# Performance work log

Measured on AMD Instinct MI355X. Metric: run time of the kernel, lower is better.

The kernel has to match this reference:

```python
import jax, jax.numpy as jnp
import numpy as np

N_NODES = 100000
N_EDGES = 1600000
N_GRAPHS = 1000
NODES_PER_GRAPH = 100
D_IN = 128
D_HID = 128
N_TASKS = 12


def setup_inputs() -> dict:
    key = jax.random.key(0)
    ks = jax.random.split(key, 6)
    X = jax.random.normal(ks[0], (N_NODES, D_IN), dtype=jnp.float32)
    edge_index = jax.random.randint(ks[1], (2, N_EDGES), 0, N_NODES, dtype=jnp.int64)
    graph_sizes = jnp.full((N_GRAPHS,), NODES_PER_GRAPH, dtype=jnp.int64)  # sums to N_NODES
    s0 = (2.0 / D_IN) ** 0.5
    W0 = jax.random.normal(ks[2], (D_IN, D_HID), dtype=jnp.float32) * s0
    b0 = jnp.zeros((D_HID,), dtype=jnp.float32)
    W1 = jax.random.normal(ks[3], (D_HID, D_HID), dtype=jnp.float32) * s0
    b1 = jnp.zeros((D_HID,), dtype=jnp.float32)
    Wf = jax.random.normal(ks[4], (D_HID, N_TASKS), dtype=jnp.float32) * s0
    bf = jnp.zeros((N_TASKS,), dtype=jnp.float32)
    return {"X": X, "edge_index": edge_index, "graph_sizes": graph_sizes,
            "W0": W0, "b0": b0, "W1": W1, "b1": b1, "Wf": Wf, "bf": bf}


def reference(X, edge_index, graph_sizes, W0, b0, W1, b1, Wf, bf):
    src, dst = edge_index[0], edge_index[1]
    n = X.shape[0]

    def gconv(x, W, b):
        # GCN-style message passing with self term: sum_{j->i} (x_j W) + x_i W + b
        xw = x @ W                                                    # [N, d]
        agg = jax.ops.segment_sum(xw[src], dst, num_segments=n)       # [N, d]
        return agg + xw + b

    # stacked conv -> relu -> dropout(eval=identity)
    h = jax.nn.relu(gconv(X, W0, b0))
    h = jax.nn.relu(gconv(h, W1, b1))
    out = jax.nn.sigmoid(h @ Wf + bf)                                  # [N, T]

    # ragged per-graph mean readout as a single segment-mean
    g = graph_sizes.shape[0]
    seg_ids = jnp.repeat(jnp.arange(g), graph_sizes, total_repeat_length=n)
    sums = jax.ops.segment_sum(out, seg_ids, num_segments=g)           # [G, T]
    return sums / graph_sizes[:, None].astype(out.dtype)
```

## Files before the change

### kernel.cpp

```cpp
#include <hip/hip_runtime.h>
#include <math.h>

#define D 128
#define NBUCK_MAX 1024
#define NB_EDGE   256
#define CAPSEG    40
#define CAPB      4096
#define CAPE      2600

typedef unsigned short u16;
typedef unsigned int   u32;
typedef __attribute__((ext_vector_type(8))) short short8;
typedef __attribute__((ext_vector_type(4))) float f32x4;
typedef __attribute__((ext_vector_type(2))) float f32x2;

static __device__ __forceinline__ u16 f32_to_bf16(float f) {
    u32 u = __builtin_bit_cast(u32, f);
    u32 r = (u + 0x7FFFu + ((u >> 16) & 1u)) >> 16;
    return (u16)r;
}
static __device__ __forceinline__ u32 pack_bf16x2(float lo, float hi) {
    return (u32)f32_to_bf16(lo) | ((u32)f32_to_bf16(hi) << 16);
}
static __device__ __forceinline__ float bf16lo_to_f32(u32 v) {
    return __builtin_bit_cast(float, v << 16);
}
static __device__ __forceinline__ float bf16hi_to_f32(u32 v) {
    return __builtin_bit_cast(float, v & 0xFFFF0000u);
}

__global__ __launch_bounds__(512) void prep_place(const int* __restrict__ src, const int* __restrict__ dst,
                                                  int E, int nbuck,
                                                  u32* __restrict__ edgeBuf, int* __restrict__ segCount,
                                                  const float* __restrict__ W0, const float* __restrict__ W1,
                                                  u16* __restrict__ Wp0, u16* __restrict__ Wp1,
                                                  const float* __restrict__ Wf, float* __restrict__ Wfp,
                                                  const int* __restrict__ gsz, int G, int* __restrict__ goff) {
    const int b = blockIdx.x;
    const int tid = threadIdx.x;
    if (b < NB_EDGE) {
        __shared__ int cur[NBUCK_MAX];
        for (int i = tid; i < nbuck; i += 512) cur[i] = 0;
        __syncthreads();
        int per = (E + NB_EDGE - 1) / NB_EDGE;
        int s = b * per, e = min(E, s + per);
        for (int i = s + tid; i < e; i += 512) {
            int d = dst[i];
            int bk = d >> 7;
            int pos = atomicAdd(&cur[bk], 1);
            if (pos < CAPSEG)
                edgeBuf[((size_t)bk * NB_EDGE + b) * CAPSEG + pos] = (u32)src[i] | ((u32)(d & 127) << 20);
        }
        __syncthreads();
        for (int i = tid; i < nbuck; i += 512) segCount[b * nbuck + i] = min(cur[i], CAPSEG);
    } else if (b == NB_EDGE) {
        __shared__ int wsum[8];
        int base = tid * 4;
        int v[4];
        #pragma unroll
        for (int k = 0; k < 4; k++) v[k] = (base + k < G) ? gsz[base + k] : 0;
        int s = v[0] + v[1] + v[2] + v[3];
        int lane = tid & 63;
        int incl = s;
        #pragma unroll
        for (int off = 1; off < 64; off <<= 1) { int t = __shfl_up(incl, off); if (lane >= off) incl += t; }
        int wv = tid >> 6;
        if (lane == 63) wsum[wv] = incl;
        __syncthreads();
        int woff = 0;
        for (int w = 0; w < wv; w++) woff += wsum[w];
        int run = woff + incl - s;
        #pragma unroll
        for (int k = 0; k < 4; k++) {
            if (base + k <= G) goff[base + k] = run;
            run += v[k];
        }
    } else if (b == NB_EDGE + 1) {
        for (int i = tid; i < 64 * 24; i += 512) {
            int lane = i / 24, r = i % 24, k = r / 3, j = r % 3;
            Wfp[i] = Wf[(((lane & 15) * 8) + k) * 12 + 3 * (lane >> 4) + j];
        }
    } else {
        int gidx = (b - (NB_EDGE + 2)) * 512 + tid;
        const float* W = (gidx < 128 * 128) ? W0 : W1;
        u16* Wp = (gidx < 128 * 128) ? Wp0 : Wp1;
        int idx = gidx & (128 * 128 - 1);
        int j = idx & 7, lane = (idx >> 3) & 63, kt = (idx >> 9) & 3, nt = idx >> 11;
        int k = kt * 32 + ((lane >> 4) << 3) + j;
        int n = nt * 16 + (lane & 15);
        Wp[idx] = f32_to_bf16(W[k * 128 + n]);
    }
}

static __device__ __forceinline__ void gemm_body(const short8 af[4], const u16* __restrict__ Wp,
                                                 u16* __restrict__ outb, int N, int row0,
                                                 int tid, int wave, int lane, int quad, int l16,
                                                 u16* Cs) {
    f32x4 acc[8];
    #pragma unroll
    for (int nt = 0; nt < 8; nt++) acc[nt] = (f32x4){0.f, 0.f, 0.f, 0.f};
    #pragma unroll
    for (int kt = 0; kt < 4; kt++) {
        #pragma unroll
        for (int nt = 0; nt < 8; nt++) {
            short8 bf = *(const short8*)(Wp + ((size_t)(nt * 4 + kt) * 64 + lane) * 8);
            acc[nt] = __builtin_amdgcn_mfma_f32_16x16x32_bf16(af[kt], bf, acc[nt], 0, 0, 0);
        }
    }
    #pragma unroll
    for (int nt = 0; nt < 8; nt++) {
        #pragma unroll
        for (int r = 0; r < 4; r++) {
            int rl = wave * 16 + quad * 4 + r;
            Cs[rl * 136 + nt * 16 + l16] = f32_to_bf16(acc[nt][r]);
        }
    }
    __syncthreads();
    for (int i = tid; i < 64 * 16; i += 256) {
        int row = i >> 4, chunk = i & 15;
        int grow = row0 + row;
        if (grow <= N)
            *(uint4*)(outb + (size_t)grow * 128 + chunk * 8) =
                *(const uint4*)(Cs + row * 136 + chunk * 8);
    }
}

__global__ __launch_bounds__(256) void finalize_gemm0(const u32* __restrict__ edgeBuf,
                                                      const int* __restrict__ segCount,
                                                      int2* __restrict__ rowse, int* __restrict__ col_idx,
                                                      int nbuck,
                                                      const float* __restrict__ A, const u16* __restrict__ Wp,
                                                      u16* __restrict__ outb, int N) {
    __shared__ u16 Cs[64 * 136];
    const int tid = threadIdx.x;
    if ((int)blockIdx.x < nbuck) {
        int* iCs   = (int*)Cs;
        u32* eL    = (u32*)iCs;
        int* hist  = iCs + CAPE;
        int* lcur  = iCs + CAPE + 128;
        int* scnt  = iCs + CAPE + 256;
        int* sbase = iCs + CAPE + 512;
        const int b = blockIdx.x;
        const size_t ebase = (size_t)b * NB_EDGE * CAPSEG;
        for (int i = tid; i < NB_EDGE; i += 256) scnt[i] = segCount[i * nbuck + b];
        if (tid < 128) hist[tid] = 0;
        __syncthreads();
        if (tid < 64) {
            int carry = 0;
            #pragma unroll
            for (int c4 = 0; c4 < NB_EDGE / 64; c4++) {
                int v = scnt[c4 * 64 + tid];
                int incl = v;
                #pragma unroll
                for (int off = 1; off < 64; off <<= 1) { int t = __shfl_up(incl, off); if (tid >= off) incl += t; }
                sbase[c4 * 64 + tid] = carry + incl - v;
                carry += __shfl(incl, 63);
            }
            if (tid == 0) sbase[NB_EDGE] = carry;
        }
        __syncthreads();
        const int nE = min(sbase[NB_EDGE], CAPE);
        for (int p = tid; p < nE; p += 256) {
            int lo = 0, hi = NB_EDGE;
            #pragma unroll
            for (int s = 0; s < 8; s++) {
                int mid = (lo + hi) >> 1;
                if (sbase[mid] <= p) lo = mid; else hi = mid;
            }
            eL[p] = edgeBuf[ebase + (size_t)lo * CAPSEG + (p - sbase[lo])];
        }
        __syncthreads();
        for (int i = tid; i < nE; i += 256)
            atomicAdd(&hist[(int)(eL[i] >> 20)], 1);
        __syncthreads();
        if (tid < 64) {
            int v0 = hist[tid * 2], v1 = hist[tid * 2 + 1];
            int s = v0 + v1;
            int incl = s;
            #pragma unroll
            for (int off = 1; off < 64; off <<= 1) { int t = __shfl_up(incl, off); if (tid >= off) incl += t; }
            int excl = incl - s;
            int le0 = excl + tid * 2;
            int le1 = le0 + v0 + 1;
            lcur[tid * 2]     = le0 + 1;
            lcur[tid * 2 + 1] = le1 + 1;
            int node = b * 128 + tid * 2;
            int st0 = b * CAPB + le0, st1 = b * CAPB + le1;
            if (node < N)     { rowse[node]     = make_int2(st0, st1);          col_idx[st0] = node; }
            if (node + 1 < N) { rowse[node + 1] = make_int2(st1, st1 + v1 + 1); col_idx[st1] = node + 1; }
        }
        __syncthreads();
        for (int i = tid; i < nE; i += 256) {
            u32 p = eL[i];
            int pos = atomicAdd(&lcur[p >> 20], 1);
            col_idx[b * CAPB + pos] = (int)(p & 0xFFFFFu);
        }
    } else {
        const int bid = blockIdx.x - nbuck;
        const int wave = tid >> 6, lane = tid & 63, quad = lane >> 4, l16 = lane & 15;
        const int row0 = bid * 64;
        const int arow = row0 + wave * 16 + l16;
        union { u32 u[4]; short8 s; } cv;
        short8 af[4];
        if (arow < N) {
            const float* ab = A + (size_t)arow * 128 + quad * 8;
            #pragma unroll
            for (int kt = 0; kt < 4; kt++) {
                float4 x0 = *(const float4*)(ab + kt * 32);
                float4 x1 = *(const float4*)(ab + kt * 32 + 4);
                cv.u[0] = pack_bf16x2(x0.x, x0.y);
                cv.u[1] = pack_bf16x2(x0.z, x0.w);
                cv.u[2] = pack_bf16x2(x1.x, x1.y);
                cv.u[3] = pack_bf16x2(x1.z, x1.w);
                af[kt] = cv.s;
            }
        } else {
            short8 z = {0, 0, 0, 0, 0, 0, 0, 0};
            #pragma unroll
            for (int kt = 0; kt < 4; kt++) af[kt] = z;
        }
        gemm_body(af, Wp, outb, N, row0, tid, wave, lane, quad, l16, Cs);
    }
}

static __device__ __forceinline__ void add_row(f32x2* acc, uint4 u) {
    acc[0] += (f32x2){bf16lo_to_f32(u.x), bf16hi_to_f32(u.x)};
    acc[1] += (f32x2){bf16lo_to_f32(u.y), bf16hi_to_f32(u.y)};
    acc[2] += (f32x2){bf16lo_to_f32(u.z), bf16hi_to_f32(u.z)};
    acc[3] += (f32x2){bf16lo_to_f32(u.w), bf16hi_to_f32(u.w)};
}

static __device__ __forceinline__ void gather2(const u16* __restrict__ xwb, const int2* __restrict__ rowse,
                                               const int* __restrict__ col_idx, const float* __restrict__ bias,
                                               int wid0, int wid1, int lane, int N, int q, int d8,
                                               float r0[8], float r1[8]) {
    f32x2 accA[4], accB[4];
    #pragma unroll
    for (int t = 0; t < 4; t++) { accA[t] = (f32x2){0.f, 0.f}; accB[t] = (f32x2){0.f, 0.f}; }
    int2 seA = rowse[wid0];
    int2 seB = rowse[wid1];
    int ia = seA.x + lane, ib = seB.x + lane;
    int jA = (ia < seA.y) ? col_idx[ia] : N;
    int jB = (ib < seB.y) ? col_idx[ib] : N;
    int cntA = __builtin_amdgcn_readfirstlane(min(64, seA.y - seA.x));
    int cntB = __builtin_amdgcn_readfirstlane(min(64, seB.y - seB.x));
    int mx = max(cntA, cntB);
    for (int i = 0; i < mx; i += 8) {
        uint4 ra0, ra1, rb0, rb1;
        const bool dA = i < cntA, dB = i < cntB;
        if (dA) {
            int a0 = __shfl(jA, i + q);
            int a1 = __shfl(jA, i + 4 + q);
            ra0 = *(const uint4*)(xwb + (size_t)a0 * D + d8);
            ra1 = *(const uint4*)(xwb + (size_t)a1 * D + d8);
        }
        if (dB) {
            int b0 = __shfl(jB, i + q);
            int b1 = __shfl(jB, i + 4 + q);
            rb0 = *(const uint4*)(xwb + (size_t)b0 * D + d8);
            rb1 = *(const uint4*)(xwb + (size_t)b1 * D + d8);
        }
        if (dA) { add_row(accA, ra0); add_row(accA, ra1); }
        if (dB) { add_row(accB, rb0); add_row(accB, rb1); }
    }
    for (int e = seA.x + 64; e < seA.y; e += 64) {
        int idx = e + lane;
        int j = (idx < seA.y) ? col_idx[idx] : N;
        int cnt = min(64, seA.y - e);
        for (int i = 0; i < cnt; i += 8) {
            int j0 = __shfl(j, i + q);
            int j1 = __shfl(j, i + 4 + q);
            add_row(accA, *(const uint4*)(xwb + (size_t)j0 * D + d8));
            add_row(accA, *(const uint4*)(xwb + (size_t)j1 * D + d8));
        }
    }
    for (int e = seB.x + 64; e < seB.y; e += 64) {
        int idx = e + lane;
        int j = (idx < seB.y) ? col_idx[idx] : N;
        int cnt = min(64, seB.y - e);
        for (int i = 0; i < cnt; i += 8) {
            int j0 = __shfl(j, i + q);
            int j1 = __shfl(j, i + 4 + q);
            add_row(accB, *(const uint4*)(xwb + (size_t)j0 * D + d8));
            add_row(accB, *(const uint4*)(xwb + (size_t)j1 * D + d8));
        }
    }

    float av0[8] = {accA[0].x, accA[0].y, accA[1].x, accA[1].y, accA[2].x, accA[2].y, accA[3].x, accA[3].y};
    float av1[8] = {accB[0].x, accB[0].y, accB[1].x, accB[1].y, accB[2].x, accB[2].y, accB[3].x, accB[3].y};
    #pragma unroll
    for (int t = 0; t < 8; t++) {
        av0[t] += __shfl_xor(av0[t], 16);
        av0[t] += __shfl_xor(av0[t], 32);
        av1[t] += __shfl_xor(av1[t], 16);
        av1[t] += __shfl_xor(av1[t], 32);
    }
    float4 ba = *(const float4*)(bias + d8);
    float4 bb = *(const float4*)(bias + d8 + 4);
    r0[0] = fmaxf(av0[0] + ba.x, 0.f);
    r0[1] = fmaxf(av0[1] + ba.y, 0.f);
    r0[2] = fmaxf(av0[2] + ba.z, 0.f);
    r0[3] = fmaxf(av0[3] + ba.w, 0.f);
    r0[4] = fmaxf(av0[4] + bb.x, 0.f);
    r0[5] = fmaxf(av0[5] + bb.y, 0.f);
    r0[6] = fmaxf(av0[6] + bb.z, 0.f);
    r0[7] = fmaxf(av0[7] + bb.w, 0.f);
    r1[0] = fmaxf(av1[0] + ba.x, 0.f);
    r1[1] = fmaxf(av1[1] + ba.y, 0.f);
    r1[2] = fmaxf(av1[2] + ba.z, 0.f);
    r1[3] = fmaxf(av1[3] + ba.w, 0.f);
    r1[4] = fmaxf(av1[4] + bb.x, 0.f);
    r1[5] = fmaxf(av1[5] + bb.y, 0.f);
    r1[6] = fmaxf(av1[6] + bb.z, 0.f);
    r1[7] = fmaxf(av1[7] + bb.w, 0.f);
}

__global__ __launch_bounds__(256) void agg_gemm1(const u16* __restrict__ xwb, const int2* __restrict__ rowse,
                                                 const int* __restrict__ col_idx, const float* __restrict__ bias,
                                                 const u16* __restrict__ Wp, u16* __restrict__ outb, int N) {
    __shared__ u16 hs[16 * 136];
    __shared__ u16 Cs[16 * 136];
    const int tid = threadIdx.x;
    const int wave = tid >> 6, lane = tid & 63, quad = lane >> 4, l16 = lane & 15;
    const int tile = blockIdx.x * 16;
    const int d8 = l16 * 8;
    #pragma unroll
    for (int m = 0; m < 4; m += 2) {
        int nl0 = wave * 4 + m, nl1 = nl0 + 1;
        int wid0 = tile + nl0, wid1 = tile + nl1;
        float r0[8], r1[8];
        int g0 = min(wid0, N - 1), g1 = min(wid1, N - 1);
        gather2(xwb, rowse, col_idx, bias, g0, g1, lane, N, quad, d8, r0, r1);
        if (quad == 0) {
            uint4 o0, o1;
            if (wid0 < N) {
                o0.x = pack_bf16x2(r0[0], r0[1]);
                o0.y = pack_bf16x2(r0[2], r0[3]);
                o0.z = pack_bf16x2(r0[4], r0[5]);
                o0.w = pack_bf16x2(r0[6], r0[7]);
            } else o0 = make_uint4(0, 0, 0, 0);
            if (wid1 < N) {
                o1.x = pack_bf16x2(r1[0], r1[1]);
                o1.y = pack_bf16x2(r1[2], r1[3]);
                o1.z = pack_bf16x2(r1[4], r1[5]);
                o1.w = pack_bf16x2(r1[6], r1[7]);
            } else o1 = make_uint4(0, 0, 0, 0);
            *(uint4*)(hs + nl0 * 136 + d8) = o0;
            *(uint4*)(hs + nl1 * 136 + d8) = o1;
        }
    }
    __syncthreads();
    short8 af[4];
    #pragma unroll
    for (int kt = 0; kt < 4; kt++)
        af[kt] = *(const short8*)(hs + l16 * 136 + kt * 32 + quad * 8);
    f32x4 acc[2];
    acc[0] = (f32x4){0.f, 0.f, 0.f, 0.f};
    acc[1] = (f32x4){0.f, 0.f, 0.f, 0.f};
    #pragma unroll
    for (int kt = 0; kt < 4; kt++) {
        #pragma unroll
        for (int t = 0; t < 2; t++) {
            int nt = wave * 2 + t;
            short8 bf = *(const short8*)(Wp + ((size_t)(nt * 4 + kt) * 64 + lane) * 8);
            acc[t] = __builtin_amdgcn_mfma_f32_16x16x32_bf16(af[kt], bf, acc[t], 0, 0, 0);
        }
    }
    #pragma unroll
    for (int t = 0; t < 2; t++) {
        int nt = wave * 2 + t;
        #pragma unroll
        for (int r = 0; r < 4; r++)
            Cs[(quad * 4 + r) * 136 + nt * 16 + l16] = f32_to_bf16(acc[t][r]);
    }
    __syncthreads();
    {
        int row = tid >> 4, chunk = tid & 15;
        int grow = tile + row;
        if (grow <= N)
            *(uint4*)(outb + (size_t)grow * 128 + chunk * 8) =
                *(const uint4*)(Cs + row * 136 + chunk * 8);
    }
}

__global__ __launch_bounds__(256) void agg_head(const u16* __restrict__ xwb, const int2* __restrict__ rowse,
                                                const int* __restrict__ col_idx, const float* __restrict__ bias,
                                                const float* __restrict__ Wfp, const float* __restrict__ bfv,
                                                float* __restrict__ out12, int N) {
    int wpair = (blockIdx.x * 256 + threadIdx.x) >> 6;
    int wid0 = wpair * 2;
    if (wid0 >= N) return;
    int wid1 = min(wid0 + 1, N - 1);
    int lane = threadIdx.x & 63;
    const int q = lane >> 4;
    const int d8 = (lane & 15) * 8;
    float w[24];
    const float* wp = Wfp + lane * 24;
    #pragma unroll
    for (int i = 0; i < 6; i++) *(float4*)(w + i * 4) = *(const float4*)(wp + i * 4);
    float r0[8], r1[8];
    gather2(xwb, rowse, col_idx, bias, wid0, wid1, lane, N, q, d8, r0, r1);
    const int t0 = 3 * q;
    float p00 = 0.f, p01 = 0.f, p02 = 0.f;
    float p10 = 0.f, p11 = 0.f, p12 = 0.f;
    #pragma unroll
    for (int k = 0; k < 8; k++) {
        p00 += r0[k] * w[k * 3];
        p01 += r0[k] * w[k * 3 + 1];
        p02 += r0[k] * w[k * 3 + 2];
        p10 += r1[k] * w[k * 3];
        p11 += r1[k] * w[k * 3 + 1];
        p12 += r1[k] * w[k * 3 + 2];
    }
    #pragma unroll
    for (int m = 1; m <= 8; m <<= 1) {
        p00 += __shfl_xor(p00, m);
        p01 += __shfl_xor(p01, m);
        p02 += __shfl_xor(p02, m);
        p10 += __shfl_xor(p10, m);
        p11 += __shfl_xor(p11, m);
        p12 += __shfl_xor(p12, m);
    }
    if ((lane & 15) == 0) {
        float b0 = bfv[t0], b1 = bfv[t0 + 1], b2 = bfv[t0 + 2];
        float* o0 = out12 + (size_t)wid0 * 12 + t0;
        o0[0] = 1.f / (1.f + __expf(-(p00 + b0)));
        o0[1] = 1.f / (1.f + __expf(-(p01 + b1)));
        o0[2] = 1.f / (1.f + __expf(-(p02 + b2)));
        if (wid0 + 1 < N) {
            float* o1 = out12 + (size_t)wid1 * 12 + t0;
            o1[0] = 1.f / (1.f + __expf(-(p10 + b0)));
            o1[1] = 1.f / (1.f + __expf(-(p11 + b1)));
            o1[2] = 1.f / (1.f + __expf(-(p12 + b2)));
        }
    }
}

__global__ __launch_bounds__(128) void graph_mean(const float* __restrict__ out12, const int* __restrict__ goff,
                                                  float* __restrict__ out, int G) {
    __shared__ float partial[120];
    int g = blockIdx.x;
    int tid = threadIdx.x;
    int start = goff[g];
    int size = goff[g + 1] - start;
    if (tid < 120) {
        int t = tid % 12, chunk = tid / 12;
        float s = 0.f;
        for (int i = chunk; i < size; i += 10)
            s += out12[(size_t)(start + i) * 12 + t];
        partial[tid] = s;
    }
    __syncthreads();
    if (tid < 12) {
        float tot = 0.f;
        #pragma unroll
        for (int c = 0; c < 10; c++) tot += partial[c * 12 + tid];
        out[(size_t)g * 12 + tid] = tot / (float)size;
    }
}


extern "C" void kernel_launch(void* const* d_in, const int* in_sizes, int n_in,
                              void* d_out, int out_size, void* d_ws, size_t ws_size,
                              hipStream_t stream) {
    const float* X   = (const float*)d_in[0];
    const int* edges = (const int*)d_in[1];
    const int* gsz   = (const int*)d_in[2];
    const float* W0  = (const float*)d_in[3];
    const float* b0  = (const float*)d_in[4];
    const float* W1  = (const float*)d_in[5];
    const float* b1  = (const float*)d_in[6];
    const float* Wf  = (const float*)d_in[7];
    const float* bfv = (const float*)d_in[8];
    float* out = (float*)d_out;

    const int N = in_sizes[0] / D;
    const int E = in_sizes[1] / 2;
    const int G = in_sizes[2];
    const int* esrc = edges;
    const int* edst = edges + E;
    const int nbuck = (N + 127) >> 7;

    char* ws = (char*)d_ws;
    char* p = ws;
    u16* xwb     = (u16*)p;  p += (((size_t)(N + 64) * D * 2) + 255) & ~255ull;
    u16* hb      = (u16*)p;  p += (((size_t)(N + 64) * D * 2) + 255) & ~255ull;
    u16* Wp0     = (u16*)p;  p += ((size_t)128 * 128 * 2 + 255) & ~255ull;
    u16* Wp1     = (u16*)p;  p += ((size_t)128 * 128 * 2 + 255) & ~255ull;
    float* Wfp   = (float*)p; p += ((size_t)64 * 24 * 4 + 255) & ~255ull;
    u32* edgeBuf = (u32*)p;  p += (((size_t)nbuck * NB_EDGE * CAPSEG * 4) + 255) & ~255ull;
    int* segCount = (int*)p; p += (((size_t)NB_EDGE * NBUCK_MAX * 4) + 255) & ~255ull;
    int* col_idx = (int*)p;  p += (((size_t)nbuck * CAPB * 4) + 255) & ~255ull;
    int2* rowse  = (int2*)p; p += (((size_t)N * 8) + 255) & ~255ull;
    float* out12 = (float*)p; p += (((size_t)N * 12 * 4) + 255) & ~255ull;
    int* goff    = (int*)p;

    prep_place<<<NB_EDGE + 2 + 64, 512, 0, stream>>>(esrc, edst, E, nbuck, edgeBuf, segCount,
                                                     W0, W1, Wp0, Wp1, Wf, Wfp, gsz, G, goff);
    const int gemmGrid = (N + 63) / 64;
    finalize_gemm0<<<nbuck + gemmGrid, 256, 0, stream>>>(edgeBuf, segCount, rowse, col_idx, nbuck,
                                                         X, Wp0, xwb, N);
    agg_gemm1<<<N / 16 + 1, 256, 0, stream>>>(xwb, rowse, col_idx, b0, Wp1, hb, N);
    const int waves2 = (N + 1) / 2;
    agg_head<<<(waves2 + 3) / 4, 256, 0, stream>>>(hb, rowse, col_idx, b1, Wfp, bfv, out12, N);
    graph_mean<<<G, 128, 0, stream>>>(out12, goff, out, G);
}
```

Before: 285.4 us.

## Compact per-chunk edge bucketing and fuse graph mean into head via atomics

Edge placement now uses larger chunks of 6144 edges. Each chunk counts its edges per destination bucket, takes a prefix scan, and writes a dense sorted payload plus a u16 offset table. This replaces the old fixed-capacity per-segment slots, which were sparse, could drop edges past capacity, and needed a separate segCount array. The per-graph mean readout is folded into agg_head: each node finds its graph by binary search and atomically adds its scaled sigmoid into the zeroed output, which removes the graph_mean kernel and the out12 round trip. In exchange, the atomic float adds make the summation order nondeterministic, and every node now performs a binary search over goff.

```diff
diff --git a/kernel.cpp b/kernel.cpp
--- a/kernel.cpp
+++ b/kernel.cpp
@@ -3,8 +3,8 @@
 
 #define D 128
 #define NBUCK_MAX 1024
-#define NB_EDGE   256
-#define CAPSEG    40
+#define PER       6144
+#define NCHUNK_PAD 512
 #define CAPB      4096
 #define CAPE      2600
 
@@ -30,35 +30,53 @@
 }
 
 __global__ __launch_bounds__(512) void prep_place(const int* __restrict__ src, const int* __restrict__ dst,
-                                                  int E, int nbuck,
-                                                  u32* __restrict__ edgeBuf, int* __restrict__ segCount,
+                                                  int E, int nbuck, int nchunk,
+                                                  u32* __restrict__ edgeBuf, u16* __restrict__ offTab,
                                                   const float* __restrict__ W0, const float* __restrict__ W1,
                                                   u16* __restrict__ Wp0, u16* __restrict__ Wp1,
                                                   const float* __restrict__ Wf, float* __restrict__ Wfp,
-                                                  const int* __restrict__ gsz, int G, int* __restrict__ goff) {
+                                                  const int* __restrict__ gsz, int G, int* __restrict__ goff,
+                                                  float* __restrict__ outZ) {
     const int b = blockIdx.x;
     const int tid = threadIdx.x;
-    if (b < NB_EDGE) {
-        __shared__ int cur[NBUCK_MAX];
-        for (int i = tid; i < nbuck; i += 512) cur[i] = 0;
-        __syncthreads();
-        int per = (E + NB_EDGE - 1) / NB_EDGE;
-        int s = b * per, e = min(E, s + per);
+    if (b < nchunk) {
+        __shared__ int cnt[NBUCK_MAX];
+        __shared__ u32 pay[PER];
+        for (int i = tid; i < nbuck; i += 512) cnt[i] = 0;
+        __syncthreads();
+        const int s = b * PER, e = min(E, s + PER);
+        for (int i = s + tid; i < e; i += 512) atomicAdd(&cnt[dst[i] >> 7], 1);
+        __syncthreads();
+        if (tid < 64) {
+            int carry = 0;
+            int rounds = (nbuck + 63) >> 6;
+            for (int r = 0; r < rounds; r++) {
+                int i = r * 64 + tid;
+                int v = (i < nbuck) ? cnt[i] : 0;
+                int incl = v;
+                #pragma unroll
+                for (int off = 1; off < 64; off <<= 1) { int t = __shfl_up(incl, off); if (tid >= off) incl += t; }
+                int excl = carry + incl - v;
+                if (i < nbuck) { offTab[(size_t)b * (NBUCK_MAX + 1) + i] = (u16)excl; cnt[i] = excl; }
+                carry += __shfl(incl, 63);
+            }
+            if (tid == 0) offTab[(size_t)b * (NBUCK_MAX + 1) + nbuck] = (u16)carry;
+        }
+        __syncthreads();
         for (int i = s + tid; i < e; i += 512) {
             int d = dst[i];
-            int bk = d >> 7;
-            int pos = atomicAdd(&cur[bk], 1);
-            if (pos < CAPSEG)
-                edgeBuf[((size_t)bk * NB_EDGE + b) * CAPSEG + pos] = (u32)src[i] | ((u32)(d & 127) << 20);
-        }
-        __syncthreads();
-        for (int i = tid; i < nbuck; i += 512) segCount[b * nbuck + i] = min(cur[i], CAPSEG);
-    } else if (b == NB_EDGE) {
+            int pos = atomicAdd(&cnt[d >> 7], 1);
+            pay[pos] = (u32)src[i] | ((u32)(d & 127) << 20);
+        }
+        __syncthreads();
+        const int m = e - s;
+        for (int i = tid; i < m; i += 512) edgeBuf[(size_t)b * PER + i] = pay[i];
+    } else if (b == nchunk) {
         __shared__ int wsum[8];
         int base = tid * 4;
         int v[4];
         #pragma unroll
-        for (int k = 0; k < 4; k++) v[k] = (base + k < G) ? gsz[base + k] : 0;
+        for (int k = 0; k < 4; k++) v[k] = (base + k < G) ? (int)gsz[base + k] : 0;
         int s = v[0] + v[1] + v[2] + v[3];
         int lane = tid & 63;
         int incl = s;
@@ -75,13 +93,14 @@
             if (base + k <= G) goff[base + k] = run;
             run += v[k];
         }
-    } else if (b == NB_EDGE + 1) {
+        for (int i = tid; i < G * 12; i += 512) outZ[i] = 0.f;
+    } else if (b == nchunk + 1) {
         for (int i = tid; i < 64 * 24; i += 512) {
             int lane = i / 24, r = i % 24, k = r / 3, j = r % 3;
             Wfp[i] = Wf[(((lane & 15) * 8) + k) * 12 + 3 * (lane >> 4) + j];
         }
     } else {
-        int gidx = (b - (NB_EDGE + 2)) * 512 + tid;
+        int gidx = (b - (nchunk + 2)) * 512 + tid;
         const float* W = (gidx < 128 * 128) ? W0 : W1;
         u16* Wp = (gidx < 128 * 128) ? Wp0 : Wp1;
         int idx = gidx & (128 * 128 - 1);
@@ -126,9 +145,9 @@
 }
 
 __global__ __launch_bounds__(256) void finalize_gemm0(const u32* __restrict__ edgeBuf,
-                                                      const int* __restrict__ segCount,
+                                                      const u16* __restrict__ offTab,
                                                       int2* __restrict__ rowse, int* __restrict__ col_idx,
-                                                      int nbuck,
+                                                      int nbuck, int nchunk,
                                                       const float* __restrict__ A, const u16* __restrict__ Wp,
                                                       u16* __restrict__ outb, int N) {
     __shared__ u16 Cs[64 * 136];
@@ -139,35 +158,41 @@
         int* hist  = iCs + CAPE;
         int* lcur  = iCs + CAPE + 128;
         int* scnt  = iCs + CAPE + 256;
-        int* sbase = iCs + CAPE + 512;
+        int* sbase = iCs + CAPE + 768;
         const int b = blockIdx.x;
-        const size_t ebase = (size_t)b * NB_EDGE * CAPSEG;
-        for (int i = tid; i < NB_EDGE; i += 256) scnt[i] = segCount[i * nbuck + b];
+        for (int c = tid; c < NCHUNK_PAD; c += 256) {
+            if (c < nchunk) {
+                int off0 = offTab[(size_t)c * (NBUCK_MAX + 1) + b];
+                int off1 = offTab[(size_t)c * (NBUCK_MAX + 1) + b + 1];
+                scnt[c] = (off0 << 16) | (off1 - off0);
+            } else scnt[c] = 0;
+        }
         if (tid < 128) hist[tid] = 0;
         __syncthreads();
         if (tid < 64) {
             int carry = 0;
             #pragma unroll
-            for (int c4 = 0; c4 < NB_EDGE / 64; c4++) {
-                int v = scnt[c4 * 64 + tid];
+            for (int c4 = 0; c4 < NCHUNK_PAD / 64; c4++) {
+                int v = scnt[c4 * 64 + tid] & 0xFFFF;
                 int incl = v;
                 #pragma unroll
                 for (int off = 1; off < 64; off <<= 1) { int t = __shfl_up(incl, off); if (tid >= off) incl += t; }
                 sbase[c4 * 64 + tid] = carry + incl - v;
                 carry += __shfl(incl, 63);
             }
-            if (tid == 0) sbase[NB_EDGE] = carry;
-        }
-        __syncthreads();
-        const int nE = min(sbase[NB_EDGE], CAPE);
+            if (tid == 0) sbase[NCHUNK_PAD] = carry;
+        }
+        __syncthreads();
+        const int nE = min(sbase[NCHUNK_PAD], CAPE);
         for (int p = tid; p < nE; p += 256) {
-            int lo = 0, hi = NB_EDGE;
+            int lo = 0, hi = NCHUNK_PAD;
             #pragma unroll
-            for (int s = 0; s < 8; s++) {
+            for (int s = 0; s < 9; s++) {
                 int mid = (lo + hi) >> 1;
                 if (sbase[mid] <= p) lo = mid; else hi = mid;
             }
-            eL[p] = edgeBuf[ebase + (size_t)lo * CAPSEG + (p - sbase[lo])];
+            int rec = scnt[lo];
+            eL[p] = edgeBuf[(size_t)lo * PER + (rec >> 16) + (p - sbase[lo])];
         }
         __syncthreads();
         for (int i = tid; i < nE; i += 256)
@@ -386,7 +411,8 @@
 __global__ __launch_bounds__(256) void agg_head(const u16* __restrict__ xwb, const int2* __restrict__ rowse,
                                                 const int* __restrict__ col_idx, const float* __restrict__ bias,
                                                 const float* __restrict__ Wfp, const float* __restrict__ bfv,
-                                                float* __restrict__ out12, int N) {
+                                                const int* __restrict__ goff, int G,
+                                                float* __restrict__ outG, int N) {
     int wpair = (blockIdx.x * 256 + threadIdx.x) >> 6;
     int wid0 = wpair * 2;
     if (wid0 >= N) return;
@@ -423,39 +449,19 @@
     }
     if ((lane & 15) == 0) {
         float b0 = bfv[t0], b1 = bfv[t0 + 1], b2 = bfv[t0 + 2];
-        float* o0 = out12 + (size_t)wid0 * 12 + t0;
-        o0[0] = 1.f / (1.f + __expf(-(p00 + b0)));
-        o0[1] = 1.f / (1.f + __expf(-(p01 + b1)));
-        o0[2] = 1.f / (1.f + __expf(-(p02 + b2)));
+        int lo = 0, hi = G;
+        while (hi - lo > 1) { int mid = (lo + hi) >> 1; if (goff[mid] <= wid0) lo = mid; else hi = mid; }
+        float inv0 = 1.f / (float)(goff[lo + 1] - goff[lo]);
+        atomicAdd(&outG[lo * 12 + t0],     inv0 / (1.f + __expf(-(p00 + b0))));
+        atomicAdd(&outG[lo * 12 + t0 + 1], inv0 / (1.f + __expf(-(p01 + b1))));
+        atomicAdd(&outG[lo * 12 + t0 + 2], inv0 / (1.f + __expf(-(p02 + b2))));
         if (wid0 + 1 < N) {
-            float* o1 = out12 + (size_t)wid1 * 12 + t0;
-            o1[0] = 1.f / (1.f + __expf(-(p10 + b0)));
-            o1[1] = 1.f / (1.f + __expf(-(p11 + b1)));
-            o1[2] = 1.f / (1.f + __expf(-(p12 + b2)));
-        }
-    }
-}
-
-__global__ __launch_bounds__(128) void graph_mean(const float* __restrict__ out12, const int* __restrict__ goff,
-                                                  float* __restrict__ out, int G) {
-    __shared__ float partial[120];
-    int g = blockIdx.x;
-    int tid = threadIdx.x;
-    int start = goff[g];
-    int size = goff[g + 1] - start;
-    if (tid < 120) {
-        int t = tid % 12, chunk = tid / 12;
-        float s = 0.f;
-        for (int i = chunk; i < size; i += 10)
-            s += out12[(size_t)(start + i) * 12 + t];
-        partial[tid] = s;
-    }
-    __syncthreads();
-    if (tid < 12) {
-        float tot = 0.f;
-        #pragma unroll
-        for (int c = 0; c < 10; c++) tot += partial[c * 12 + tid];
-        out[(size_t)g * 12 + tid] = tot / (float)size;
+            int g1 = (wid1 < goff[lo + 1]) ? lo : lo + 1;
+            float inv1 = 1.f / (float)(goff[g1 + 1] - goff[g1]);
+            atomicAdd(&outG[g1 * 12 + t0],     inv1 / (1.f + __expf(-(p10 + b0))));
+            atomicAdd(&outG[g1 * 12 + t0 + 1], inv1 / (1.f + __expf(-(p11 + b1))));
+            atomicAdd(&outG[g1 * 12 + t0 + 2], inv1 / (1.f + __expf(-(p12 + b2))));
+        }
     }
 }
 
@@ -480,6 +486,7 @@
     const int* esrc = edges;
     const int* edst = edges + E;
     const int nbuck = (N + 127) >> 7;
+    const int nchunk = (E + PER - 1) / PER;
 
     char* ws = (char*)d_ws;
     char* p = ws;
@@ -488,20 +495,18 @@
     u16* Wp0     = (u16*)p;  p += ((size_t)128 * 128 * 2 + 255) & ~255ull;
     u16* Wp1     = (u16*)p;  p += ((size_t)128 * 128 * 2 + 255) & ~255ull;
     float* Wfp   = (float*)p; p += ((size_t)64 * 24 * 4 + 255) & ~255ull;
-    u32* edgeBuf = (u32*)p;  p += (((size_t)nbuck * NB_EDGE * CAPSEG * 4) + 255) & ~255ull;
-    int* segCount = (int*)p; p += (((size_t)NB_EDGE * NBUCK_MAX * 4) + 255) & ~255ull;
+    u32* edgeBuf = (u32*)p;  p += (((size_t)nchunk * PER * 4) + 255) & ~255ull;
+    u16* offTab  = (u16*)p;  p += (((size_t)nchunk * (NBUCK_MAX + 1) * 2) + 255) & ~255ull;
     int* col_idx = (int*)p;  p += (((size_t)nbuck * CAPB * 4) + 255) & ~255ull;
     int2* rowse  = (int2*)p; p += (((size_t)N * 8) + 255) & ~255ull;
-    float* out12 = (float*)p; p += (((size_t)N * 12 * 4) + 255) & ~255ull;
     int* goff    = (int*)p;
 
-    prep_place<<<NB_EDGE + 2 + 64, 512, 0, stream>>>(esrc, edst, E, nbuck, edgeBuf, segCount,
-                                                     W0, W1, Wp0, Wp1, Wf, Wfp, gsz, G, goff);
+    prep_place<<<nchunk + 2 + 64, 512, 0, stream>>>(esrc, edst, E, nbuck, nchunk, edgeBuf, offTab,
+                                                    W0, W1, Wp0, Wp1, Wf, Wfp, gsz, G, goff, out);
     const int gemmGrid = (N + 63) / 64;
-    finalize_gemm0<<<nbuck + gemmGrid, 256, 0, stream>>>(edgeBuf, segCount, rowse, col_idx, nbuck,
+    finalize_gemm0<<<nbuck + gemmGrid, 256, 0, stream>>>(edgeBuf, offTab, rowse, col_idx, nbuck, nchunk,
                                                          X, Wp0, xwb, N);
     agg_gemm1<<<N / 16 + 1, 256, 0, stream>>>(xwb, rowse, col_idx, b0, Wp1, hb, N);
     const int waves2 = (N + 1) / 2;
-    agg_head<<<(waves2 + 3) / 4, 256, 0, stream>>>(hb, rowse, col_idx, b1, Wfp, bfv, out12, N);
-    graph_mean<<<G, 128, 0, stream>>>(out12, goff, out, G);
-}
+    agg_head<<<(waves2 + 3) / 4, 256, 0, stream>>>(hb, rowse, col_idx, b1, Wfp, bfv, goff, G, out, N);
+}
```

Result: slower. 350.5 us (+22.8%).
